# Optimization experiments

Hardware: AMD Instinct MI355X
Metric: run time of the kernel (lower is better)

The kernel has to match this reference:

```python
import jax, jax.numpy as jnp
import numpy as np

NUM_HEADS = 4

def transpose_qkv(X, H):
    # (bs, num_p, nn, d) -> (bs*H, num_p, nn, d//H)
    bs, num_p, nnb, d = X.shape
    X = X.reshape(bs, num_p, nnb, H, d // H).transpose(0, 3, 1, 2, 4)
    return X.reshape(bs * H, num_p, nnb, d // H)

def transpose_output(X, H):
    # (bs*H, num_p, hd) -> (bs, num_p, H*hd)
    bH, num_p, hd = X.shape
    X = X.reshape(bH // H, H, num_p, hd).transpose(0, 2, 1, 3)
    return X.reshape(bH // H, num_p, H * hd)

def setup_inputs() -> dict:
    key = jax.random.key(0)
    ks = jax.random.split(key, 8)
    bs, num_p, fea_dim = 4, 16384, 64
    hd = fea_dim // NUM_HEADS  # hidden_size = 16
    q = jax.random.normal(ks[0], (bs, num_p, 1, fea_dim), jnp.float32)
    k = jax.random.normal(ks[1], (bs, num_p, 9, fea_dim), jnp.float32)
    v = jax.random.normal(ks[2], (bs, num_p, 9, fea_dim), jnp.float32)
    pos_encoding = jax.random.normal(ks[3], (bs, num_p, 9, fea_dim), jnp.float32)
    W1 = jax.random.normal(ks[4], (hd, hd * 4), jnp.float32) * (1.0 / np.sqrt(hd))
    b1 = jnp.zeros((hd * 4,), jnp.float32)
    W2 = jax.random.normal(ks[5], (hd * 4, hd), jnp.float32) * (1.0 / np.sqrt(hd * 4))
    b2 = jnp.zeros((hd,), jnp.float32)
    return {"q": q, "k": k, "v": v, "pos_encoding": pos_encoding,
            "W1": W1, "b1": b1, "W2": W2, "b2": b2}

def reference(q, k, v, pos_encoding, W1, b1, W2, b2):
    H = NUM_HEADS
    qh = transpose_qkv(q, H)              # (bs*H, num_p, 1, hd)
    kh = transpose_qkv(k, H)              # (bs*H, num_p, 9, hd)
    vh = transpose_qkv(v, H)
    ph = transpose_qkv(pos_encoding, H)
    x = qh - kh + ph                       # broadcast over neighbor dim -> (bs*H, num_p, 9, hd)
    scores = jax.nn.relu(x @ W1 + b1) @ W2 + b2  # per-channel attention logits
    attn = jax.nn.softmax(scores, axis=-2)       # softmax over 9 neighbors, per channel
    out = jnp.einsum('bijd,bijd->bid', attn, vh + ph)  # (bs*H, num_p, hd)
    return transpose_output(out, H)        # (bs, num_p, fea_dim)
```

## Files before the change

### kernel.cpp

```cpp
#include <hip/hip_runtime.h>

typedef unsigned int uint;
typedef unsigned short ushort;
typedef __attribute__((ext_vector_type(2))) uint  u32x2;
typedef __attribute__((ext_vector_type(4))) short s16x4;
typedef __attribute__((ext_vector_type(4))) float f32x4;

#if __has_builtin(__builtin_amdgcn_mfma_f32_16x16x16bf16_1k)
#define MFMA(a,b,c) __builtin_amdgcn_mfma_f32_16x16x16bf16_1k((a),(b),(c),0,0,0)
#else
__device__ __forceinline__ f32x4 mfma_fb(s16x4 a, s16x4 b, f32x4 c){
    asm volatile("v_mfma_f32_16x16x16_bf16 %0, %1, %2, %0\n\ts_nop 7\n\ts_nop 7"
                 : "+v"(c) : "v"(a), "v"(b));
    return c;
}
#define MFMA(a,b,c) mfma_fb((a),(b),(c))
#endif

__device__ __forceinline__ uint  fbits(float f){ return __builtin_bit_cast(uint, f); }
__device__ __forceinline__ float ibits(uint u){ return __builtin_bit_cast(float, u); }

__device__ __forceinline__ void split4(f32x4 x, s16x4& hi, s16x4& lo){
    uint b0=fbits(x.x), b1=fbits(x.y), b2=fbits(x.z), b3=fbits(x.w);
    u32x2 h; h.x = (b0>>16) | (b1 & 0xFFFF0000u); h.y = (b2>>16) | (b3 & 0xFFFF0000u);
    float l0 = x.x - ibits(b0 & 0xFFFF0000u);
    float l1 = x.y - ibits(b1 & 0xFFFF0000u);
    float l2 = x.z - ibits(b2 & 0xFFFF0000u);
    float l3 = x.w - ibits(b3 & 0xFFFF0000u);
    u32x2 l; l.x = (fbits(l0)>>16) | (fbits(l1) & 0xFFFF0000u);
    l.y = (fbits(l2)>>16) | (fbits(l3) & 0xFFFF0000u);
    hi = __builtin_bit_cast(s16x4, h);
    lo = __builtin_bit_cast(s16x4, l);
}

__global__ void pack_weights(const float* __restrict__ W1, const float* __restrict__ b1,
                             const float* __restrict__ W2, float* __restrict__ ws)
{
    const int e = threadIdx.x;
    const int t = e >> 6, l = e & 63;
    const int g = l >> 4, m = l & 15;

    float w1v[4], w2v[4];
    #pragma unroll
    for (int j = 0; j < 4; ++j) {
        w1v[j] = W1[(4*g + j)*64 + 16*t + m];
        w2v[j] = W2[(16*t + 4*g + j)*16 + m];
    }
    ushort h1[4], o1[4], h2[4], o2[4];
    #pragma unroll
    for (int j = 0; j < 4; ++j) {
        uint u1 = fbits(w1v[j]);
        ushort a = (ushort)((u1 + 0x7FFFu + ((u1>>16)&1u)) >> 16);
        float  r = w1v[j] - ibits(((uint)a) << 16);
        uint ur = fbits(r);
        ushort b = (ushort)((ur + 0x7FFFu + ((ur>>16)&1u)) >> 16);
        h1[j] = a; o1[j] = b;
        uint u2 = fbits(w2v[j]);
        a = (ushort)((u2 + 0x7FFFu + ((u2>>16)&1u)) >> 16);
        r = w2v[j] - ibits(((uint)a) << 16);
        ur = fbits(r);
        b = (ushort)((ur + 0x7FFFu + ((ur>>16)&1u)) >> 16);
        h2[j] = a; o2[j] = b;
    }
    u32x2* wp = (u32x2*)ws;
    u32x2 x;
    x.x = (uint)h1[0] | ((uint)h1[1] << 16); x.y = (uint)h1[2] | ((uint)h1[3] << 16);
    wp[e] = x;
    x.x = (uint)o1[0] | ((uint)o1[1] << 16); x.y = (uint)o1[2] | ((uint)o1[3] << 16);
    wp[256 + e] = x;
    x.x = (uint)h2[0] | ((uint)h2[1] << 16); x.y = (uint)h2[2] | ((uint)h2[3] << 16);
    wp[512 + e] = x;
    x.x = (uint)o2[0] | ((uint)o2[1] << 16); x.y = (uint)o2[2] | ((uint)o2[3] << 16);
    wp[768 + e] = x;

    f32x4 bb;
    bb.x = b1[16*t + 4*g + 0]; bb.y = b1[16*t + 4*g + 1];
    bb.z = b1[16*t + 4*g + 2]; bb.w = b1[16*t + 4*g + 3];
    ((f32x4*)(ws + 2048))[e] = bb;
}

__global__ __launch_bounds__(256) __attribute__((amdgpu_waves_per_eu(4, 4)))
void subattn_mfma(const float* __restrict__ q, const float* __restrict__ k,
                  const float* __restrict__ v, const float* __restrict__ pe,
                  const float* __restrict__ ws, float* __restrict__ out)
{
    const int tid = threadIdx.x;
    const int wv  = tid >> 6;
    const int l   = tid & 63;
    const int n   = l & 15, g = l >> 4;
    const int grp = blockIdx.x * 4 + wv;
    const int rg  = grp * 16 + n;
    const int bp  = rg >> 2, h = rg & 3;

    const u32x2* wp = (const u32x2*)ws;
    const f32x4* bptr = (const f32x4*)(ws + 2048);
    s16x4 w1h[4], w1l[4], w2h[4], w2l[4];
    f32x4 b1f[4];
    #pragma unroll
    for (int t = 0; t < 4; ++t) {
        w1h[t] = __builtin_bit_cast(s16x4, wp[      t*64 + l]);
        w1l[t] = __builtin_bit_cast(s16x4, wp[256 + t*64 + l]);
        w2h[t] = __builtin_bit_cast(s16x4, wp[512 + t*64 + l]);
        w2l[t] = __builtin_bit_cast(s16x4, wp[768 + t*64 + l]);
        b1f[t] = bptr[t*64 + l];
    }

    const size_t qoff  = (size_t)rg * 16 + g * 4;
    const f32x4  qf    = *(const f32x4*)(q + qoff);
    const size_t kbase = (size_t)bp * 576 + h * 16 + g * 4;

    f32x4 lsum = {0.f, 0.f, 0.f, 0.f};
    f32x4 acc  = {0.f, 0.f, 0.f, 0.f};

    f32x4 kf = *(const f32x4*)(k  + kbase);
    f32x4 pf = *(const f32x4*)(pe + kbase);

    for (int j = 0; j < 9; ++j) {
        f32x4 kn, pn;
        if (j < 8) {
            const size_t noff = kbase + (size_t)(j + 1) * 64;
            kn = *(const f32x4*)(k  + noff);
            pn = *(const f32x4*)(pe + noff);
        }
        const f32x4 vf = *(const f32x4*)(v + kbase + (size_t)j * 64);

        f32x4 x = qf - kf + pf;
        s16x4 xh, xl; split4(x, xh, xl);

        f32x4 c2a = {0.f, 0.f, 0.f, 0.f};
        f32x4 c2b = {0.f, 0.f, 0.f, 0.f};
        #pragma unroll
        for (int tp = 0; tp < 2; ++tp) {
            const int t0 = tp * 2, t1 = tp * 2 + 1;
            f32x4 c1a = b1f[t0], c1b = b1f[t1];
            c1a = MFMA(w1l[t0], xh, c1a);  c1b = MFMA(w1l[t1], xh, c1b);
            c1a = MFMA(w1h[t0], xl, c1a);  c1b = MFMA(w1h[t1], xl, c1b);
            c1a = MFMA(w1h[t0], xh, c1a);  c1b = MFMA(w1h[t1], xh, c1b);
            f32x4 ra, rb;
            ra.x = fmaxf(c1a.x, 0.f); ra.y = fmaxf(c1a.y, 0.f);
            ra.z = fmaxf(c1a.z, 0.f); ra.w = fmaxf(c1a.w, 0.f);
            rb.x = fmaxf(c1b.x, 0.f); rb.y = fmaxf(c1b.y, 0.f);
            rb.z = fmaxf(c1b.z, 0.f); rb.w = fmaxf(c1b.w, 0.f);
            s16x4 hah, hal, hbh, hbl;
            split4(ra, hah, hal);
            split4(rb, hbh, hbl);
            c2a = MFMA(w2l[t0], hah, c2a);  c2b = MFMA(w2l[t1], hbh, c2b);
            c2a = MFMA(w2h[t0], hal, c2a);  c2b = MFMA(w2h[t1], hbl, c2b);
            c2a = MFMA(w2h[t0], hah, c2a);  c2b = MFMA(w2h[t1], hbh, c2b);
        }
        const f32x4 c2 = c2a + c2b;

        const f32x4 vp = vf + pf;
        float e0 = __expf(c2.x), e1 = __expf(c2.y);
        float e2 = __expf(c2.z), e3 = __expf(c2.w);
        lsum.x += e0; lsum.y += e1; lsum.z += e2; lsum.w += e3;
        acc.x = fmaf(e0, vp.x, acc.x); acc.y = fmaf(e1, vp.y, acc.y);
        acc.z = fmaf(e2, vp.z, acc.z); acc.w = fmaf(e3, vp.w, acc.w);

        kf = kn; pf = pn;
    }

    f32x4 o;
    o.x = __fdividef(acc.x, lsum.x); o.y = __fdividef(acc.y, lsum.y);
    o.z = __fdividef(acc.z, lsum.z); o.w = __fdividef(acc.w, lsum.w);
    *(f32x4*)(out + qoff) = o;
}

extern "C" void kernel_launch(void* const* d_in, const int* in_sizes, int n_in,
                              void* d_out, int out_size, void* d_ws, size_t ws_size,
                              hipStream_t stream) {
    const float* q  = (const float*)d_in[0];
    const float* k  = (const float*)d_in[1];
    const float* v  = (const float*)d_in[2];
    const float* pe = (const float*)d_in[3];
    const float* W1 = (const float*)d_in[4];
    const float* b1 = (const float*)d_in[5];
    const float* W2 = (const float*)d_in[6];
    float* out = (float*)d_out;
    float* ws  = (float*)d_ws;

    pack_weights<<<1, 256, 0, stream>>>(W1, b1, W2, ws);

    const int nrows  = in_sizes[0] / 16;
    const int groups = nrows / 16;
    const int grid   = groups / 4;
    subattn_mfma<<<grid, 256, 0, stream>>>(q, k, v, pe, ws, out);
}
```

Before: 104.4 us.

## Use 16x16x32 bf16 MFMA with reduced split-precision for attention MLP

Replaces the 16x16x16 bf16 MFMA with the gfx950 16x16x32 variant and packs the weight operands into 8-element vectors. The first layer keeps a two-term weight split (hi and lo packed along K) with single-term bf16 activations, and the second layer drops the split entirely, going from 12 MFMAs to 6 per neighbor. Activation conversion uses the hardware v_cvt_pk_bf16_f32 instruction instead of manual bit splitting. The aim is to cut MFMA and VALU work per neighbor, at the cost of lower precision in the scores, which could break accuracy tolerance.

```diff
diff --git a/kernel.cpp b/kernel.cpp
--- a/kernel.cpp
+++ b/kernel.cpp
@@ -2,81 +2,71 @@
 
 typedef unsigned int uint;
 typedef unsigned short ushort;
-typedef __attribute__((ext_vector_type(2))) uint  u32x2;
-typedef __attribute__((ext_vector_type(4))) short s16x4;
-typedef __attribute__((ext_vector_type(4))) float f32x4;
+typedef __attribute__((ext_vector_type(4))) uint   u32x4;
+typedef __attribute__((ext_vector_type(8))) short  short8;
+typedef __attribute__((ext_vector_type(8))) __bf16 bf16x8;
+typedef __attribute__((ext_vector_type(4))) float  f32x4;
 
-#if __has_builtin(__builtin_amdgcn_mfma_f32_16x16x16bf16_1k)
-#define MFMA(a,b,c) __builtin_amdgcn_mfma_f32_16x16x16bf16_1k((a),(b),(c),0,0,0)
+__device__ __forceinline__ f32x4 mfma32(short8 a, short8 b, f32x4 c){
+#if __has_builtin(__builtin_amdgcn_mfma_f32_16x16x32_bf16)
+    return __builtin_amdgcn_mfma_f32_16x16x32_bf16(
+        __builtin_bit_cast(bf16x8, a), __builtin_bit_cast(bf16x8, b), c, 0, 0, 0);
 #else
-__device__ __forceinline__ f32x4 mfma_fb(s16x4 a, s16x4 b, f32x4 c){
-    asm volatile("v_mfma_f32_16x16x16_bf16 %0, %1, %2, %0\n\ts_nop 7\n\ts_nop 7"
+    asm volatile("v_mfma_f32_16x16x32_bf16 %0, %1, %2, %0\n\ts_nop 7\n\ts_nop 7"
                  : "+v"(c) : "v"(a), "v"(b));
     return c;
+#endif
 }
-#define MFMA(a,b,c) mfma_fb((a),(b),(c))
-#endif
 
 __device__ __forceinline__ uint  fbits(float f){ return __builtin_bit_cast(uint, f); }
 __device__ __forceinline__ float ibits(uint u){ return __builtin_bit_cast(float, u); }
-
-__device__ __forceinline__ void split4(f32x4 x, s16x4& hi, s16x4& lo){
-    uint b0=fbits(x.x), b1=fbits(x.y), b2=fbits(x.z), b3=fbits(x.w);
-    u32x2 h; h.x = (b0>>16) | (b1 & 0xFFFF0000u); h.y = (b2>>16) | (b3 & 0xFFFF0000u);
-    float l0 = x.x - ibits(b0 & 0xFFFF0000u);
-    float l1 = x.y - ibits(b1 & 0xFFFF0000u);
-    float l2 = x.z - ibits(b2 & 0xFFFF0000u);
-    float l3 = x.w - ibits(b3 & 0xFFFF0000u);
-    u32x2 l; l.x = (fbits(l0)>>16) | (fbits(l1) & 0xFFFF0000u);
-    l.y = (fbits(l2)>>16) | (fbits(l3) & 0xFFFF0000u);
-    hi = __builtin_bit_cast(s16x4, h);
-    lo = __builtin_bit_cast(s16x4, l);
+__device__ __forceinline__ ushort rne_bf16(float f){
+    uint u = fbits(f);
+    return (ushort)((u + 0x7FFFu + ((u >> 16) & 1u)) >> 16);
+}
+__device__ __forceinline__ uint cvtpk(float a, float b){
+    uint r;
+    asm("v_cvt_pk_bf16_f32 %0, %1, %2" : "=v"(r) : "v"(a), "v"(b));
+    return r;
 }
 
 __global__ void pack_weights(const float* __restrict__ W1, const float* __restrict__ b1,
                              const float* __restrict__ W2, float* __restrict__ ws)
 {
-    const int e = threadIdx.x;
-    const int t = e >> 6, l = e & 63;
+    const int e4 = threadIdx.x;
+    const int t = e4 >> 6, l = e4 & 63;
     const int g = l >> 4, m = l & 15;
+    uint* wsu = (uint*)ws;
 
-    float w1v[4], w2v[4];
+    ushort el[8];
     #pragma unroll
-    for (int j = 0; j < 4; ++j) {
-        w1v[j] = W1[(4*g + j)*64 + 16*t + m];
-        w2v[j] = W2[(16*t + 4*g + j)*16 + m];
+    for (int i = 0; i < 8; ++i) {
+        const int c = 4*g + (i & 3);
+        const float w = W1[c * 64 + 16*t + m];
+        const ushort hi = rne_bf16(w);
+        if (i < 4) el[i] = hi;
+        else       el[i] = rne_bf16(w - ibits(((uint)hi) << 16));
     }
-    ushort h1[4], o1[4], h2[4], o2[4];
     #pragma unroll
-    for (int j = 0; j < 4; ++j) {
-        uint u1 = fbits(w1v[j]);
-        ushort a = (ushort)((u1 + 0x7FFFu + ((u1>>16)&1u)) >> 16);
-        float  r = w1v[j] - ibits(((uint)a) << 16);
-        uint ur = fbits(r);
-        ushort b = (ushort)((ur + 0x7FFFu + ((ur>>16)&1u)) >> 16);
-        h1[j] = a; o1[j] = b;
-        uint u2 = fbits(w2v[j]);
-        a = (ushort)((u2 + 0x7FFFu + ((u2>>16)&1u)) >> 16);
-        r = w2v[j] - ibits(((uint)a) << 16);
-        ur = fbits(r);
-        b = (ushort)((ur + 0x7FFFu + ((ur>>16)&1u)) >> 16);
-        h2[j] = a; o2[j] = b;
+    for (int r = 0; r < 4; ++r)
+        wsu[(t*64 + l)*4 + r] = (uint)el[2*r] | ((uint)el[2*r+1] << 16);
+
+    if (t < 2) {
+        const int p = t;
+        ushort e2[8];
+        #pragma unroll
+        for (int i = 0; i < 8; ++i) {
+            const int hid = 16*(2*p + (i >> 2)) + 4*g + (i & 3);
+            e2[i] = rne_bf16(W2[hid * 16 + m]);
+        }
+        #pragma unroll
+        for (int r = 0; r < 4; ++r)
+            wsu[1024 + (p*64 + l)*4 + r] = (uint)e2[2*r] | ((uint)e2[2*r+1] << 16);
     }
-    u32x2* wp = (u32x2*)ws;
-    u32x2 x;
-    x.x = (uint)h1[0] | ((uint)h1[1] << 16); x.y = (uint)h1[2] | ((uint)h1[3] << 16);
-    wp[e] = x;
-    x.x = (uint)o1[0] | ((uint)o1[1] << 16); x.y = (uint)o1[2] | ((uint)o1[3] << 16);
-    wp[256 + e] = x;
-    x.x = (uint)h2[0] | ((uint)h2[1] << 16); x.y = (uint)h2[2] | ((uint)h2[3] << 16);
-    wp[512 + e] = x;
-    x.x = (uint)o2[0] | ((uint)o2[1] << 16); x.y = (uint)o2[2] | ((uint)o2[3] << 16);
-    wp[768 + e] = x;
 
-    f32x4 bb;
-    bb.x = b1[16*t + 4*g + 0]; bb.y = b1[16*t + 4*g + 1];
-    bb.z = b1[16*t + 4*g + 2]; bb.w = b1[16*t + 4*g + 3];
-    ((f32x4*)(ws + 2048))[e] = bb;
+    #pragma unroll
+    for (int r = 0; r < 4; ++r)
+        ws[1536 + (t*64 + l)*4 + r] = b1[16*t + 4*g + r];
 }
 
 __global__ __launch_bounds__(256) __attribute__((amdgpu_waves_per_eu(4, 4)))
@@ -92,18 +82,18 @@
     const int rg  = grp * 16 + n;
     const int bp  = rg >> 2, h = rg & 3;
 
-    const u32x2* wp = (const u32x2*)ws;
-    const f32x4* bptr = (const f32x4*)(ws + 2048);
-    s16x4 w1h[4], w1l[4], w2h[4], w2l[4];
-    f32x4 b1f[4];
+    const u32x4* a1p = (const u32x4*)ws;
+    const u32x4* a2p = (const u32x4*)(ws + 1024);
+    const f32x4* bfp = (const f32x4*)(ws + 1536);
+    short8 a1[4], a2[2];
+    f32x4  b1f[4];
     #pragma unroll
     for (int t = 0; t < 4; ++t) {
-        w1h[t] = __builtin_bit_cast(s16x4, wp[      t*64 + l]);
-        w1l[t] = __builtin_bit_cast(s16x4, wp[256 + t*64 + l]);
-        w2h[t] = __builtin_bit_cast(s16x4, wp[512 + t*64 + l]);
-        w2l[t] = __builtin_bit_cast(s16x4, wp[768 + t*64 + l]);
-        b1f[t] = bptr[t*64 + l];
+        a1[t]  = __builtin_bit_cast(short8, a1p[t*64 + l]);
+        b1f[t] = bfp[t*64 + l];
     }
+    #pragma unroll
+    for (int p = 0; p < 2; ++p) a2[p] = __builtin_bit_cast(short8, a2p[p*64 + l]);
 
     const size_t qoff  = (size_t)rg * 16 + g * 4;
     const f32x4  qf    = *(const f32x4*)(q + qoff);
@@ -124,35 +114,38 @@
         }
         const f32x4 vf = *(const f32x4*)(v + kbase + (size_t)j * 64);
 
-        f32x4 x = qf - kf + pf;
-        s16x4 xh, xl; split4(x, xh, xl);
+        const f32x4 x = qf - kf + pf;
+        const uint xp0 = cvtpk(x.x, x.y);
+        const uint xp1 = cvtpk(x.z, x.w);
+        const u32x4 bxu = {xp0, xp1, xp0, xp1};
+        const short8 bx = __builtin_bit_cast(short8, bxu);
 
-        f32x4 c2a = {0.f, 0.f, 0.f, 0.f};
-        f32x4 c2b = {0.f, 0.f, 0.f, 0.f};
-        #pragma unroll
-        for (int tp = 0; tp < 2; ++tp) {
-            const int t0 = tp * 2, t1 = tp * 2 + 1;
-            f32x4 c1a = b1f[t0], c1b = b1f[t1];
-            c1a = MFMA(w1l[t0], xh, c1a);  c1b = MFMA(w1l[t1], xh, c1b);
-            c1a = MFMA(w1h[t0], xl, c1a);  c1b = MFMA(w1h[t1], xl, c1b);
-            c1a = MFMA(w1h[t0], xh, c1a);  c1b = MFMA(w1h[t1], xh, c1b);
-            f32x4 ra, rb;
-            ra.x = fmaxf(c1a.x, 0.f); ra.y = fmaxf(c1a.y, 0.f);
-            ra.z = fmaxf(c1a.z, 0.f); ra.w = fmaxf(c1a.w, 0.f);
-            rb.x = fmaxf(c1b.x, 0.f); rb.y = fmaxf(c1b.y, 0.f);
-            rb.z = fmaxf(c1b.z, 0.f); rb.w = fmaxf(c1b.w, 0.f);
-            s16x4 hah, hal, hbh, hbl;
-            split4(ra, hah, hal);
-            split4(rb, hbh, hbl);
-            c2a = MFMA(w2l[t0], hah, c2a);  c2b = MFMA(w2l[t1], hbh, c2b);
-            c2a = MFMA(w2h[t0], hal, c2a);  c2b = MFMA(w2h[t1], hbl, c2b);
-            c2a = MFMA(w2h[t0], hah, c2a);  c2b = MFMA(w2h[t1], hbh, c2b);
+        f32x4 c1_0 = mfma32(a1[0], bx, b1f[0]);
+        f32x4 c1_1 = mfma32(a1[1], bx, b1f[1]);
+        f32x4 c1_2 = mfma32(a1[2], bx, b1f[2]);
+        f32x4 c1_3 = mfma32(a1[3], bx, b1f[3]);
+
+        uint ph[4][2];
+        {
+            f32x4 c1s[4] = {c1_0, c1_1, c1_2, c1_3};
+            #pragma unroll
+            for (int t = 0; t < 4; ++t) {
+                const float r0 = fmaxf(c1s[t].x, 0.f), r1 = fmaxf(c1s[t].y, 0.f);
+                const float r2 = fmaxf(c1s[t].z, 0.f), r3 = fmaxf(c1s[t].w, 0.f);
+                ph[t][0] = cvtpk(r0, r1);
+                ph[t][1] = cvtpk(r2, r3);
+            }
         }
-        const f32x4 c2 = c2a + c2b;
+
+        const u32x4 bh0u = {ph[0][0], ph[0][1], ph[1][0], ph[1][1]};
+        const u32x4 bh1u = {ph[2][0], ph[2][1], ph[3][0], ph[3][1]};
+        f32x4 c2 = {0.f, 0.f, 0.f, 0.f};
+        c2 = mfma32(a2[0], __builtin_bit_cast(short8, bh0u), c2);
+        c2 = mfma32(a2[1], __builtin_bit_cast(short8, bh1u), c2);
 
         const f32x4 vp = vf + pf;
-        float e0 = __expf(c2.x), e1 = __expf(c2.y);
-        float e2 = __expf(c2.z), e3 = __expf(c2.w);
+        const float e0 = __expf(c2.x), e1 = __expf(c2.y);
+        const float e2 = __expf(c2.z), e3 = __expf(c2.w);
         lsum.x += e0; lsum.y += e1; lsum.z += e2; lsum.w += e3;
         acc.x = fmaf(e0, vp.x, acc.x); acc.y = fmaf(e1, vp.y, acc.y);
         acc.z = fmaf(e2, vp.z, acc.z); acc.w = fmaf(e3, vp.w, acc.w);
```

New measurement: 98.37 us. 5.8% less time.
